# Optimization experiments

Hardware: AMD Instinct MI355X
Metric: run time of the kernel (lower is better)

## Reference

```python
import jax, jax.numpy as jnp
import numpy as np

B, T, D = 4, 2048, 768
H = 12
DH = D // H
DFF = 3072
EPS = 1e-5


def _layernorm(x, g, b):
    mu = jnp.mean(x, axis=-1, keepdims=True)
    var = jnp.var(x, axis=-1, keepdims=True)
    return (x - mu) * jax.lax.rsqrt(var + EPS) * g + b


def setup_inputs() -> dict:
    key = jax.random.key(0)
    ks = jax.random.split(key, 12)
    s = lambda fan_in: 1.0 / np.sqrt(fan_in)
    return {
        "x": jax.random.normal(ks[0], (B, T, D), dtype=jnp.float32),
        "ln1_g": jnp.ones((D,), jnp.float32),
        "ln1_b": jnp.zeros((D,), jnp.float32),
        "w_qkv": jax.random.uniform(ks[1], (D, 3 * D), jnp.float32, -s(D), s(D)),
        "b_qkv": jax.random.uniform(ks[2], (3 * D,), jnp.float32, -s(D), s(D)),
        "w_proj": jax.random.uniform(ks[3], (D, D), jnp.float32, -s(D), s(D)),
        "b_proj": jax.random.uniform(ks[4], (D,), jnp.float32, -s(D), s(D)),
        "ln2_g": jnp.ones((D,), jnp.float32),
        "ln2_b": jnp.zeros((D,), jnp.float32),
        "w_ff1": jax.random.uniform(ks[5], (D, DFF), jnp.float32, -s(D), s(D)),
        "b_ff1": jax.random.uniform(ks[6], (DFF,), jnp.float32, -s(D), s(D)),
        "w_ff2": jax.random.uniform(ks[7], (DFF, D), jnp.float32, -s(DFF), s(DFF)),
        "b_ff2": jax.random.uniform(ks[8], (D,), jnp.float32, -s(DFF), s(DFF)),
    }


def reference(x, ln1_g, ln1_b, w_qkv, b_qkv, w_proj, b_proj,
              ln2_g, ln2_b, w_ff1, b_ff1, w_ff2, b_ff2):
    # --- attention sublayer ---
    h = _layernorm(x, ln1_g, ln1_b)
    qkv = h @ w_qkv + b_qkv                       # [B,T,3D]
    q, k, v = jnp.split(qkv, 3, axis=-1)
    q = q.reshape(B, T, H, DH).transpose(0, 2, 1, 3)  # [B,H,T,DH]
    k = k.reshape(B, T, H, DH).transpose(0, 2, 1, 3)
    v = v.reshape(B, T, H, DH).transpose(0, 2, 1, 3)
    att = jnp.einsum('bhqd,bhkd->bhqk', q, k) / jnp.sqrt(jnp.float32(DH))
    causal = jnp.tril(jnp.ones((T, T), dtype=bool))
    att = jnp.where(causal, att, -jnp.inf)
    att = jax.nn.softmax(att, axis=-1)
    out = jnp.einsum('bhqk,bhkd->bhqd', att, v)    # [B,H,T,DH]
    out = out.transpose(0, 2, 1, 3).reshape(B, T, D)
    x = x + out @ w_proj + b_proj
    # --- MLP sublayer ---
    h2 = _layernorm(x, ln2_g, ln2_b)
    h2 = jax.nn.gelu(h2 @ w_ff1 + b_ff1, approximate=False)
    x = x + h2 @ w_ff2 + b_ff2
    return x
```

## Files before the change

### kernel.cpp

```cpp
#include <hip/hip_runtime.h>
#include <cstdint>
#include <cstddef>

typedef unsigned short u16;
typedef unsigned int u32;
typedef __attribute__((ext_vector_type(8))) short s16x8;
typedef __attribute__((ext_vector_type(4))) float f32x4;

#define NB 4
#define NT 2048
#define ND 768
#define NH 12
#define NDH 64
#define NFF 3072
#define NM (NB*NT)

__device__ __forceinline__ u16 f2b(float f){
  union { float f; unsigned u; } c; c.f = f;
  unsigned r = c.u + 0x7fffu + ((c.u >> 16) & 1u);
  return (u16)(r >> 16);
}

__device__ __forceinline__ f32x4 mfma16(s16x8 a, s16x8 b, f32x4 c){
  return __builtin_amdgcn_mfma_f32_16x16x32_bf16(a, b, c, 0, 0, 0);
}

__device__ __forceinline__ void stage16(u16* lds, const u16* g){
  __builtin_amdgcn_global_load_lds(
      (const __attribute__((address_space(1))) unsigned int*)g,
      (__attribute__((address_space(3))) unsigned int*)lds,
      16, 0, 0);
}

__device__ __forceinline__ float gelu_f(float v){
  const float x = v * 0.70710678118654752f;
  const float ax = fabsf(x);
  const float t = 1.f / (1.f + 0.3275911f * ax);
  const float y = t * (0.254829592f + t * (-0.284496736f + t * (1.421413741f
                + t * (-1.453152027f + t * 1.061405429f))));
  float er = 1.f - y * __expf(-ax * ax);
  er = copysignf(er, x);
  return 0.5f * v * (1.f + er);
}

__global__ __launch_bounds__(256) void transpose_bf16(
    const float* __restrict__ in, u16* __restrict__ out, int K, int N)
{
  __shared__ float tile[32][33];
  const int n0 = blockIdx.x * 32, k0 = blockIdx.y * 32;
  const int tx = threadIdx.x, ty = threadIdx.y;
  #pragma unroll
  for (int i = 0; i < 32; i += 8)
    tile[ty + i][tx] = in[(size_t)(k0 + ty + i) * N + n0 + tx];
  __syncthreads();
  #pragma unroll
  for (int i = 0; i < 32; i += 8)
    out[(size_t)(n0 + ty + i) * K + k0 + tx] = f2b(tile[tx][ty + i]);
}

__global__ __launch_bounds__(256) void ln_kernel(
    const float* __restrict__ x, const float* __restrict__ g,
    const float* __restrict__ b, u16* __restrict__ out)
{
  const int row = blockIdx.x;
  const int t = threadIdx.x;
  const float* xr = x + (size_t)row * ND;
  float v0 = xr[t], v1 = xr[t + 256], v2 = xr[t + 512];
  float s = v0 + v1 + v2;
  float ss = v0*v0 + v1*v1 + v2*v2;
  #pragma unroll
  for (int o = 32; o; o >>= 1) { s += __shfl_xor(s, o, 64); ss += __shfl_xor(ss, o, 64); }
  __shared__ float red[8];
  const int w = t >> 6;
  if ((t & 63) == 0) { red[w] = s; red[4 + w] = ss; }
  __syncthreads();
  s  = red[0] + red[1] + red[2] + red[3];
  ss = red[4] + red[5] + red[6] + red[7];
  const float mu = s * (1.f / ND);
  const float var = ss * (1.f / ND) - mu * mu;
  const float rinv = rsqrtf(var + 1e-5f);
  u16* orow = out + (size_t)row * ND;
  orow[t]       = f2b((v0 - mu) * rinv * g[t]       + b[t]);
  orow[t + 256] = f2b((v1 - mu) * rinv * g[t + 256] + b[t + 256]);
  orow[t + 512] = f2b((v2 - mu) * rinv * g[t + 512] + b[t + 512]);
}

template<int EPI>
__global__ __launch_bounds__(512, 2) void gemm256(
    const u16* __restrict__ A, const u16* __restrict__ Bt,
    const float* __restrict__ bias,
    void* __restrict__ o0, void* __restrict__ o1, void* __restrict__ o2,
    const int N, const int K)
{
  __shared__ u16 Al[2][16384];
  __shared__ u16 Bl[2][16384];
  const int tid = threadIdx.x;
  const int lane = tid & 63, wid = tid >> 6;
  const int wm = wid >> 2, wn = wid & 3;
  const int lg = lane >> 4, lm = lane & 15;

  const int nwg = gridDim.x * gridDim.y;
  int bid = blockIdx.y * gridDim.x + blockIdx.x;
  bid = (bid & 7) * (nwg >> 3) + (bid >> 3);
  const int bm = (bid % gridDim.x) * 256;
  const int bn = (bid / gridDim.x) * 256;

  f32x4 acc[8][4] = {};

  const int srow = (wid << 4) + (lane >> 2);
  const int schunk = (lane & 3) ^ ((lane >> 3) & 3);
  const u16* Ap = A  + (size_t)(bm + srow) * K + schunk * 8;
  const u16* Bp = Bt + (size_t)(bn + srow) * K + schunk * 8;
  const int wlds = wid << 9;

  const int nkt = K >> 6;

  auto STAGE = [&](int kt2) {
    const int buf = kt2 & 1;
    const size_t kof = (size_t)(kt2 << 6);
    #pragma unroll
    for (int h = 0; h < 2; ++h)
      #pragma unroll
      for (int L2 = 0; L2 < 2; ++L2) {
        const size_t gofs = (size_t)(L2 << 7) * K + kof + (h << 5);
        const int lofs = h * 8192 + L2 * 4096 + wlds;
        stage16(&Al[buf][lofs], Ap + gofs);
        stage16(&Bl[buf][lofs], Bp + gofs);
      }
  };

  auto LDA = [&](int buf, int rf, int ks) -> s16x8 {
    const int r = (wm << 7) + (rf << 4) + lm;
    const int s = lg ^ ((lm >> 1) & 3);
    return *(const s16x8*)&Al[buf][(ks << 13) + (r << 5) + (s << 3)];
  };
  auto LDB = [&](int buf, int cf, int ks) -> s16x8 {
    const int r = (wn << 6) + (cf << 4) + lm;
    const int s = lg ^ ((lm >> 1) & 3);
    return *(const s16x8*)&Bl[buf][(ks << 13) + (r << 5) + (s << 3)];
  };

  STAGE(0);

  for (int kt = 0; kt < nkt; ++kt) {
    const int buf = kt & 1;
    asm volatile("s_waitcnt vmcnt(0)" ::: "memory");
    __builtin_amdgcn_s_barrier();

    s16x8 a0[4][2], b0[2][2];
    #pragma unroll
    for (int i = 0; i < 4; ++i) { a0[i][0] = LDA(buf, i, 0); a0[i][1] = LDA(buf, i, 1); }
    #pragma unroll
    for (int j = 0; j < 2; ++j) { b0[j][0] = LDB(buf, j, 0); b0[j][1] = LDB(buf, j, 1); }
    if (kt + 1 < nkt) STAGE(kt + 1);
    __builtin_amdgcn_s_barrier();
    __builtin_amdgcn_s_setprio(1);
    #pragma unroll
    for (int i = 0; i < 4; ++i)
      #pragma unroll
      for (int j = 0; j < 2; ++j) {
        acc[i][j] = mfma16(a0[i][0], b0[j][0], acc[i][j]);
        acc[i][j] = mfma16(a0[i][1], b0[j][1], acc[i][j]);
      }
    __builtin_amdgcn_s_setprio(0);
    __builtin_amdgcn_s_barrier();

    s16x8 b1[2][2];
    #pragma unroll
    for (int j = 0; j < 2; ++j) { b1[j][0] = LDB(buf, 2 + j, 0); b1[j][1] = LDB(buf, 2 + j, 1); }
    __builtin_amdgcn_s_barrier();
    __builtin_amdgcn_s_setprio(1);
    #pragma unroll
    for (int i = 0; i < 4; ++i)
      #pragma unroll
      for (int j = 0; j < 2; ++j) {
        acc[i][2 + j] = mfma16(a0[i][0], b1[j][0], acc[i][2 + j]);
        acc[i][2 + j] = mfma16(a0[i][1], b1[j][1], acc[i][2 + j]);
      }
    __builtin_amdgcn_s_setprio(0);
    __builtin_amdgcn_s_barrier();

    s16x8 a1[4][2];
    #pragma unroll
    for (int i = 0; i < 4; ++i) { a1[i][0] = LDA(buf, 4 + i, 0); a1[i][1] = LDA(buf, 4 + i, 1); }
    __builtin_amdgcn_s_barrier();
    __builtin_amdgcn_s_setprio(1);
    #pragma unroll
    for (int i = 0; i < 4; ++i)
      #pragma unroll
      for (int j = 0; j < 2; ++j) {
        acc[4 + i][2 + j] = mfma16(a1[i][0], b1[j][0], acc[4 + i][2 + j]);
        acc[4 + i][2 + j] = mfma16(a1[i][1], b1[j][1], acc[4 + i][2 + j]);
      }
    __builtin_amdgcn_s_setprio(0);
    __builtin_amdgcn_s_barrier();

    __builtin_amdgcn_s_setprio(1);
    #pragma unroll
    for (int i = 0; i < 4; ++i)
      #pragma unroll
      for (int j = 0; j < 2; ++j) {
        acc[4 + i][j] = mfma16(a1[i][0], b0[j][0], acc[4 + i][j]);
        acc[4 + i][j] = mfma16(a1[i][1], b0[j][1], acc[4 + i][j]);
      }
    __builtin_amdgcn_s_setprio(0);
  }

  #pragma unroll
  for (int i = 0; i < 8; ++i)
    #pragma unroll
    for (int j = 0; j < 4; ++j) {
      const int col = bn + (wn << 6) + (j << 4) + lm;
      const float bb = bias[col];
      #pragma unroll
      for (int r = 0; r < 4; ++r) {
        const int row = bm + (wm << 7) + (i << 4) + (lg << 2) + r;
        float v = acc[i][j][r] + bb;
        if (EPI == 0) {
          u16* dst; int rem;
          if (col < ND)            { dst = (u16*)o0; rem = col; v *= 0.125f; }
          else if (col < 2 * ND)   { dst = (u16*)o1; rem = col - ND; }
          else                     { dst = (u16*)o2; rem = col - 2 * ND; }
          const int hh = rem >> 6, dh = rem & 63;
          const int bb2 = row >> 11, tt = row & 2047;
          dst[(((size_t)bb2 * NH + hh) * NT + tt) * NDH + dh] = f2b(v);
        } else {
          ((u16*)o0)[(size_t)row * NFF + col] = f2b(gelu_f(v));
        }
      }
    }
}

template<int EPI>
__global__ __launch_bounds__(256, 4) void gemm_bt(
    const u16* __restrict__ A, const u16* __restrict__ Bt,
    const float* __restrict__ bias, const float* __restrict__ res,
    void* __restrict__ o0, const int M, const int N, const int K)
{
  __shared__ u16 As[3][64 * 32];
  __shared__ u16 Bs[3][128 * 32];
  const int tid = threadIdx.x;
  const int lane = tid & 63, wid = tid >> 6;
  const int wr = wid >> 1, wc = wid & 1;
  const int lg = lane >> 4, lm = lane & 15;
  const int bm = blockIdx.x * 64, bn = blockIdx.y * 128;

  f32x4 acc[2][4] = {};

  const int srow = tid >> 2;
  const int schunk = (tid & 3) ^ ((tid >> 3) & 3);
  const u16* ApT = A  + (size_t)(bm + srow) * K + schunk * 8;
  const u16* BpT = Bt + (size_t)(bn + srow) * K + schunk * 8;
  const size_t rs64 = (size_t)64 * K;
  const int woff = wid * 512;
  const int fswz = (lm >> 1) & 3;

  const int nt = K >> 5;

  #pragma unroll
  for (int p = 0; p < 2; ++p) {
    const int k0 = p << 5;
    stage16(&As[p][woff], ApT + k0);
    stage16(&Bs[p][woff],        BpT + k0);
    stage16(&Bs[p][woff + 2048], BpT + rs64 + k0);
  }

  for (int t = 0; t < nt; ++t) {
    if (t < nt - 1) asm volatile("s_waitcnt vmcnt(3)" ::: "memory");
    else            asm volatile("s_waitcnt vmcnt(0)" ::: "memory");
    __builtin_amdgcn_s_barrier();
    __builtin_amdgcn_sched_barrier(0);
    if (t + 2 < nt) {
      const int k0 = (t + 2) << 5;
      const int wb = (t + 2) % 3;
      stage16(&As[wb][woff], ApT + k0);
      stage16(&Bs[wb][woff],        BpT + k0);
      stage16(&Bs[wb][woff + 2048], BpT + rs64 + k0);
    }
    __builtin_amdgcn_sched_barrier(0);
    const int rb = t % 3;
    s16x8 af[2], bf[4];
    #pragma unroll
    for (int i = 0; i < 2; i++)
      af[i] = *(const s16x8*)&As[rb][(wr * 32 + i * 16 + lm) * 32 + ((lg ^ fswz) * 8)];
    #pragma unroll
    for (int j = 0; j < 4; j++)
      bf[j] = *(const s16x8*)&Bs[rb][(wc * 64 + j * 16 + lm) * 32 + ((lg ^ fswz) * 8)];
    #pragma unroll
    for (int i = 0; i < 2; i++)
      #pragma unroll
      for (int j = 0; j < 4; j++)
        acc[i][j] = mfma16(af[i], bf[j], acc[i][j]);
  }

  #pragma unroll
  for (int i = 0; i < 2; i++)
    #pragma unroll
    for (int j = 0; j < 4; j++) {
      const int col = bn + wc * 64 + j * 16 + lm;
      const float bb = bias[col];
      #pragma unroll
      for (int r = 0; r < 4; r++) {
        const int row = bm + wr * 32 + i * 16 + lg * 4 + r;
        const float v = acc[i][j][r] + bb;
        ((float*)o0)[(size_t)row * ND + col] = v + res[(size_t)row * ND + col];
      }
    }
}

__global__ __launch_bounds__(256,2) void attn_kernel(
    const u16* __restrict__ Q, const u16* __restrict__ Kg,
    const u16* __restrict__ V, u16* __restrict__ O)
{
  const int pairIdx = blockIdx.y;
  const int bh = blockIdx.x;
  const int b = bh / NH, h = bh % NH;
  const int tid = threadIdx.x;
  const int lane = tid & 63, w = tid >> 6;
  const int lg = lane >> 4, lm = lane & 15;
  const int sr = tid >> 3;
  const int sc = (tid & 7) * 8;

  __shared__ u16 Ks[64 * 64];
  __shared__ u16 Vt[64 * 64];
  __shared__ u16 Ps[4][16 * 64];

  const u16* Qb = Q  + (size_t)bh * NT * NDH;
  const u16* Kb = Kg + (size_t)bh * NT * NDH;
  const u16* Vb = V  + (size_t)bh * NT * NDH;

  for (int half = 0; half < 2; ++half) {
    const int si = half ? (31 - pairIdx) : pairIdx;
    const int q0 = si * 64;
    const int ktmax = si;

    const s16x8 qf0 = *(const s16x8*)&Qb[(size_t)(q0 + w * 16 + lm) * NDH + lg * 8];
    const s16x8 qf1 = *(const s16x8*)&Qb[(size_t)(q0 + w * 16 + lm) * NDH + 32 + lg * 8];

    f32x4 oacc[4] = {};
    float m = -INFINITY, l = 0.f;

    s16x8 kva = *(const s16x8*)&Kb[(size_t)sr * NDH + sc];
    s16x8 kvb = *(const s16x8*)&Kb[(size_t)(sr + 32) * NDH + sc];
    s16x8 vva = *(const s16x8*)&Vb[(size_t)sr * NDH + sc];
    s16x8 vvb = *(const s16x8*)&Vb[(size_t)(sr + 32) * NDH + sc];

    for (int kt = 0; kt <= ktmax; ++kt) {
      __syncthreads();
      *(s16x8*)&Ks[sr * 64 + (sc ^ ((sr & 7) << 3))] = kva;
      *(s16x8*)&Ks[(sr + 32) * 64 + (sc ^ ((sr & 7) << 3))] = kvb;
      #pragma unroll
      for (int e = 0; e < 8; ++e)
        Vt[(sc + e) * 64 + (sr ^ ((tid & 7) << 3))] = (u16)vva[e];
      #pragma unroll
      for (int e = 0; e < 8; ++e)
        Vt[(sc + e) * 64 + ((sr + 32) ^ ((tid & 7) << 3))] = (u16)vvb[e];
      __syncthreads();

      if (kt < ktmax) {
        const u16* Kn = Kb + (size_t)(kt + 1) * 64 * NDH;
        const u16* Vn = Vb + (size_t)(kt + 1) * 64 * NDH;
        kva = *(const s16x8*)&Kn[(size_t)sr * NDH + sc];
        kvb = *(const s16x8*)&Kn[(size_t)(sr + 32) * NDH + sc];
        vva = *(const s16x8*)&Vn[(size_t)sr * NDH + sc];
        vvb = *(const s16x8*)&Vn[(size_t)(sr + 32) * NDH + sc];
      }

      f32x4 sv[4];
      #pragma unroll
      for (int n = 0; n < 4; ++n) {
        const int krow = (n * 16 + lm) * 64;
        const int swz = (lm & 7) << 3;
        s16x8 kf0 = *(const s16x8*)&Ks[krow + ((lg * 8) ^ swz)];
        s16x8 kf1 = *(const s16x8*)&Ks[krow + ((32 + lg * 8) ^ swz)];
        f32x4 s4 = {};
        s4 = mfma16(kf0, qf0, s4);
        s4 = mfma16(kf1, qf1, s4);
        sv[n] = s4;
      }

      if (kt == ktmax) {
        #pragma unroll
        for (int n = 0; n < 4; ++n)
          #pragma unroll
          for (int r = 0; r < 4; ++r)
            if (n * 16 + lg * 4 + r > w * 16 + lm) sv[n][r] = -INFINITY;
      }

      float mx = -INFINITY;
      #pragma unroll
      for (int n = 0; n < 4; ++n)
        #pragma unroll
        for (int r = 0; r < 4; ++r) mx = fmaxf(mx, sv[n][r]);
      mx = fmaxf(mx, __shfl_xor(mx, 16));
      mx = fmaxf(mx, __shfl_xor(mx, 32));
      const float mnew = fmaxf(m, mx);
      const float alpha = __expf(m - mnew);
      m = mnew;

      float rs = 0.f;
      u32 pk[4][2];
      #pragma unroll
      for (int n = 0; n < 4; ++n) {
        const float p0 = __expf(sv[n][0] - mnew);
        const float p1 = __expf(sv[n][1] - mnew);
        const float p2 = __expf(sv[n][2] - mnew);
        const float p3 = __expf(sv[n][3] - mnew);
        rs += (p0 + p1) + (p2 + p3);
        pk[n][0] = (u32)f2b(p0) | ((u32)f2b(p1) << 16);
        pk[n][1] = (u32)f2b(p2) | ((u32)f2b(p3) << 16);
      }
      rs += __shfl_xor(rs, 16);
      rs += __shfl_xor(rs, 32);
      l = l * alpha + rs;

      #pragma unroll
      for (int n = 0; n < 4; ++n) {
        const int idx0 = lm * 64 + ((n * 16 + lg * 4) ^ ((lm & 7) << 3));
        *(u32*)&Ps[w][idx0] = pk[n][0];
        *(u32*)&Ps[w][idx0 + 2] = pk[n][1];
      }

      float av[4];
      #pragma unroll
      for (int r = 0; r < 4; ++r) av[r] = __shfl(alpha, lg * 4 + r);
      #pragma unroll
      for (int d = 0; d < 4; ++d)
        #pragma unroll
        for (int r = 0; r < 4; ++r) oacc[d][r] *= av[r];

      #pragma unroll
      for (int kh = 0; kh < 2; ++kh) {
        const s16x8 pf = *(const s16x8*)&Ps[w][lm * 64 + ((kh * 32 + lg * 8) ^ ((lm & 7) << 3))];
        #pragma unroll
        for (int dt = 0; dt < 4; ++dt) {
          const int g = (2 * dt + (lm >> 3)) & 7;
          const s16x8 vf = *(const s16x8*)&Vt[(dt * 16 + lm) * 64 + (((kh * 4 + lg) ^ g) << 3)];
          oacc[dt] = mfma16(pf, vf, oacc[dt]);
        }
      }
    }

    float lv[4];
    #pragma unroll
    for (int r = 0; r < 4; ++r) lv[r] = 1.f / __shfl(l, lg * 4 + r);
    #pragma unroll
    for (int dt = 0; dt < 4; ++dt)
      #pragma unroll
      for (int r = 0; r < 4; ++r) {
        const int qg = q0 + w * 16 + lg * 4 + r;
        O[((size_t)b * NT + qg) * ND + h * NDH + dt * 16 + lm] = f2b(oacc[dt][r] * lv[r]);
      }
  }
}

extern "C" void kernel_launch(void* const* d_in, const int* in_sizes, int n_in,
                              void* d_out, int out_size, void* d_ws, size_t ws_size,
                              hipStream_t stream)
{
  const float* x      = (const float*)d_in[0];
  const float* ln1_g  = (const float*)d_in[1];
  const float* ln1_b  = (const float*)d_in[2];
  const float* w_qkv  = (const float*)d_in[3];
  const float* b_qkv  = (const float*)d_in[4];
  const float* w_proj = (const float*)d_in[5];
  const float* b_proj = (const float*)d_in[6];
  const float* ln2_g  = (const float*)d_in[7];
  const float* ln2_b  = (const float*)d_in[8];
  const float* w_ff1  = (const float*)d_in[9];
  const float* b_ff1  = (const float*)d_in[10];
  const float* w_ff2  = (const float*)d_in[11];
  const float* b_ff2  = (const float*)d_in[12];

  char* ws = (char*)d_ws;
  u16*   wt_qkv = (u16*)(ws + 0);
  u16*   wt_proj= (u16*)(ws + 3538944);
  u16*   wt_ff1 = (u16*)(ws + 4718592);
  u16*   wt_ff2 = (u16*)(ws + 9437184);
  u16*   hbuf   = (u16*)(ws + 14155776);
  u16*   qbuf   = (u16*)(ws + 26738688);
  u16*   kbuf   = (u16*)(ws + 39321600);
  u16*   vbuf   = (u16*)(ws + 51904512);
  u16*   aobuf  = (u16*)(ws + 64487424);
  float* x1     = (float*)(ws + 77070336);
  u16*   h2buf  = (u16*)(ws + 102236160);
  u16*   ff1buf = hbuf;

  transpose_bf16<<<dim3(2304/32,  768/32), dim3(32,8), 0, stream>>>(w_qkv,  wt_qkv,  768, 2304);
  transpose_bf16<<<dim3( 768/32,  768/32), dim3(32,8), 0, stream>>>(w_proj, wt_proj, 768,  768);
  transpose_bf16<<<dim3(3072/32,  768/32), dim3(32,8), 0, stream>>>(w_ff1,  wt_ff1,  768, 3072);
  transpose_bf16<<<dim3( 768/32, 3072/32), dim3(32,8), 0, stream>>>(w_ff2,  wt_ff2, 3072,  768);

  ln_kernel<<<NM, 256, 0, stream>>>(x, ln1_g, ln1_b, hbuf);
  gemm256<0><<<dim3(NM/256, 2304/256), 512, 0, stream>>>(hbuf, wt_qkv, b_qkv,
                                                         qbuf, kbuf, vbuf, 2304, ND);
  attn_kernel<<<dim3(NB*NH, 16), 256, 0, stream>>>(qbuf, kbuf, vbuf, aobuf);
  gemm_bt<1><<<dim3(NM/64, ND/128), 256, 0, stream>>>(aobuf, wt_proj, b_proj, x,
                                                      x1, NM, ND, ND);
  ln_kernel<<<NM, 256, 0, stream>>>(x1, ln2_g, ln2_b, h2buf);
  gemm256<2><<<dim3(NM/256, NFF/256), 512, 0, stream>>>(h2buf, wt_ff1, b_ff1,
                                                        ff1buf, nullptr, nullptr, NFF, ND);
  gemm_bt<3><<<dim3(NM/64, ND/128), 256, 0, stream>>>(ff1buf, wt_ff2, b_ff2, x1,
                                                      d_out, NM, ND, NFF);
}
```

Measured before the change: 339.8 us.

## Pipeline gemm256 staging per k-half, fuse weight transposes, fix Vt bank conflicts

The 256x256 GEMM main loop now splits each k-tile into two 32-wide halves. Global-to-LDS stages for A and B of the next tile are interleaved between MFMA phases, with partial vmcnt waits in place of a full drain each iteration. Bias values are preloaded before the loop. The four weight-transpose launches are merged into one kernel, and the attention V-transpose swizzle now folds in the element index to reduce LDS bank conflicts on stores and reads. Together these aim to cut load stalls, launch overhead and LDS conflicts, at the cost of more complex wait-count bookkeeping that must stay correct.

Result: faster. 326.5 us (-3.9%).

```diff
diff --git a/kernel.cpp b/kernel.cpp
--- a/kernel.cpp
+++ b/kernel.cpp
@@ -43,11 +43,21 @@
   return 0.5f * v * (1.f + er);
 }
 
-__global__ __launch_bounds__(256) void transpose_bf16(
-    const float* __restrict__ in, u16* __restrict__ out, int K, int N)
+__global__ __launch_bounds__(256) void transpose_all(
+    const float* __restrict__ w_qkv, const float* __restrict__ w_proj,
+    const float* __restrict__ w_ff1, const float* __restrict__ w_ff2,
+    u16* __restrict__ o_qkv, u16* __restrict__ o_proj,
+    u16* __restrict__ o_ff1, u16* __restrict__ o_ff2)
 {
+  int bid = blockIdx.x;
+  const float* in; u16* out; int K, N, nx;
+  if (bid < 1728)      { in = w_qkv;  out = o_qkv;  K = 768;  N = 2304; nx = 72; }
+  else if ((bid -= 1728) < 576)  { in = w_proj; out = o_proj; K = 768;  N = 768;  nx = 24; }
+  else if ((bid -= 576) < 2304)  { in = w_ff1;  out = o_ff1;  K = 768;  N = 3072; nx = 96; }
+  else { bid -= 2304;              in = w_ff2;  out = o_ff2;  K = 3072; N = 768;  nx = 24; }
+  const int n0 = (bid % nx) * 32, k0 = (bid / nx) * 32;
+
   __shared__ float tile[32][33];
-  const int n0 = blockIdx.x * 32, k0 = blockIdx.y * 32;
   const int tx = threadIdx.x, ty = threadIdx.y;
   #pragma unroll
   for (int i = 0; i < 32; i += 8)
@@ -115,20 +125,18 @@
 
   const int nkt = K >> 6;
 
-  auto STAGE = [&](int kt2) {
+  auto STAGE_A = [&](int kt2, int h) {
     const int buf = kt2 & 1;
-    const size_t kof = (size_t)(kt2 << 6);
-    #pragma unroll
-    for (int h = 0; h < 2; ++h)
-      #pragma unroll
-      for (int L2 = 0; L2 < 2; ++L2) {
-        const size_t gofs = (size_t)(L2 << 7) * K + kof + (h << 5);
-        const int lofs = h * 8192 + L2 * 4096 + wlds;
-        stage16(&Al[buf][lofs], Ap + gofs);
-        stage16(&Bl[buf][lofs], Bp + gofs);
-      }
+    const size_t kof = (size_t)(kt2 << 6) + (h << 5);
+    stage16(&Al[buf][h * 8192 + wlds],        Ap + kof);
+    stage16(&Al[buf][h * 8192 + 4096 + wlds], Ap + (size_t)128 * K + kof);
   };
-
+  auto STAGE_B = [&](int kt2, int h) {
+    const int buf = kt2 & 1;
+    const size_t kof = (size_t)(kt2 << 6) + (h << 5);
+    stage16(&Bl[buf][h * 8192 + wlds],        Bp + kof);
+    stage16(&Bl[buf][h * 8192 + 4096 + wlds], Bp + (size_t)128 * K + kof);
+  };
   auto LDA = [&](int buf, int rf, int ks) -> s16x8 {
     const int r = (wm << 7) + (rf << 4) + lm;
     const int s = lg ^ ((lm >> 1) & 3);
@@ -140,70 +148,79 @@
     return *(const s16x8*)&Bl[buf][(ks << 13) + (r << 5) + (s << 3)];
   };
 
-  STAGE(0);
+  float bb[4];
+  #pragma unroll
+  for (int j = 0; j < 4; ++j) bb[j] = bias[bn + (wn << 6) + (j << 4) + lm];
+  asm volatile("s_waitcnt vmcnt(0)" ::: "memory");
+
+  STAGE_A(0, 0); STAGE_B(0, 0); STAGE_A(0, 1); STAGE_B(0, 1);
+  asm volatile("s_waitcnt vmcnt(4)" ::: "memory");
+  __builtin_amdgcn_s_barrier();
+  __builtin_amdgcn_sched_barrier(0);
 
   for (int kt = 0; kt < nkt; ++kt) {
     const int buf = kt & 1;
-    asm volatile("s_waitcnt vmcnt(0)" ::: "memory");
-    __builtin_amdgcn_s_barrier();
-
-    s16x8 a0[4][2], b0[2][2];
-    #pragma unroll
-    for (int i = 0; i < 4; ++i) { a0[i][0] = LDA(buf, i, 0); a0[i][1] = LDA(buf, i, 1); }
-    #pragma unroll
-    for (int j = 0; j < 2; ++j) { b0[j][0] = LDB(buf, j, 0); b0[j][1] = LDB(buf, j, 1); }
-    if (kt + 1 < nkt) STAGE(kt + 1);
+    const bool more = (kt + 1 < nkt);
+    s16x8 a[8], b0, b1;
+
+    #pragma unroll
+    for (int i = 0; i < 8; ++i) a[i] = LDA(buf, i, 0);
+    b0 = LDB(buf, 0, 0); b1 = LDB(buf, 1, 0);
+    if (more) STAGE_A(kt + 1, 0);
     __builtin_amdgcn_s_barrier();
     __builtin_amdgcn_s_setprio(1);
     #pragma unroll
-    for (int i = 0; i < 4; ++i)
-      #pragma unroll
-      for (int j = 0; j < 2; ++j) {
-        acc[i][j] = mfma16(a0[i][0], b0[j][0], acc[i][j]);
-        acc[i][j] = mfma16(a0[i][1], b0[j][1], acc[i][j]);
-      }
+    for (int i = 0; i < 8; ++i) {
+      acc[i][0] = mfma16(a[i], b0, acc[i][0]);
+      acc[i][1] = mfma16(a[i], b1, acc[i][1]);
+    }
     __builtin_amdgcn_s_setprio(0);
     __builtin_amdgcn_s_barrier();
 
-    s16x8 b1[2][2];
-    #pragma unroll
-    for (int j = 0; j < 2; ++j) { b1[j][0] = LDB(buf, 2 + j, 0); b1[j][1] = LDB(buf, 2 + j, 1); }
+    b0 = LDB(buf, 2, 0); b1 = LDB(buf, 3, 0);
+    if (more) STAGE_B(kt + 1, 0);
     __builtin_amdgcn_s_barrier();
     __builtin_amdgcn_s_setprio(1);
     #pragma unroll
-    for (int i = 0; i < 4; ++i)
-      #pragma unroll
-      for (int j = 0; j < 2; ++j) {
-        acc[i][2 + j] = mfma16(a0[i][0], b1[j][0], acc[i][2 + j]);
-        acc[i][2 + j] = mfma16(a0[i][1], b1[j][1], acc[i][2 + j]);
-      }
+    for (int i = 0; i < 8; ++i) {
+      acc[i][2] = mfma16(a[i], b0, acc[i][2]);
+      acc[i][3] = mfma16(a[i], b1, acc[i][3]);
+    }
     __builtin_amdgcn_s_setprio(0);
-    __builtin_amdgcn_s_barrier();
-
-    s16x8 a1[4][2];
-    #pragma unroll
-    for (int i = 0; i < 4; ++i) { a1[i][0] = LDA(buf, 4 + i, 0); a1[i][1] = LDA(buf, 4 + i, 1); }
+    if (more) asm volatile("s_waitcnt vmcnt(4)" ::: "memory");
+    else      asm volatile("s_waitcnt vmcnt(0)" ::: "memory");
+    __builtin_amdgcn_s_barrier();
+    __builtin_amdgcn_sched_barrier(0);
+
+    #pragma unroll
+    for (int i = 0; i < 8; ++i) a[i] = LDA(buf, i, 1);
+    b0 = LDB(buf, 0, 1); b1 = LDB(buf, 1, 1);
+    if (more) STAGE_A(kt + 1, 1);
     __builtin_amdgcn_s_barrier();
     __builtin_amdgcn_s_setprio(1);
     #pragma unroll
-    for (int i = 0; i < 4; ++i)
-      #pragma unroll
-      for (int j = 0; j < 2; ++j) {
-        acc[4 + i][2 + j] = mfma16(a1[i][0], b1[j][0], acc[4 + i][2 + j]);
-        acc[4 + i][2 + j] = mfma16(a1[i][1], b1[j][1], acc[4 + i][2 + j]);
-      }
+    for (int i = 0; i < 8; ++i) {
+      acc[i][0] = mfma16(a[i], b0, acc[i][0]);
+      acc[i][1] = mfma16(a[i], b1, acc[i][1]);
+    }
     __builtin_amdgcn_s_setprio(0);
     __builtin_amdgcn_s_barrier();
 
+    b0 = LDB(buf, 2, 1); b1 = LDB(buf, 3, 1);
+    if (more) STAGE_B(kt + 1, 1);
+    __builtin_amdgcn_s_barrier();
     __builtin_amdgcn_s_setprio(1);
     #pragma unroll
-    for (int i = 0; i < 4; ++i)
-      #pragma unroll
-      for (int j = 0; j < 2; ++j) {
-        acc[4 + i][j] = mfma16(a1[i][0], b0[j][0], acc[4 + i][j]);
-        acc[4 + i][j] = mfma16(a1[i][1], b0[j][1], acc[4 + i][j]);
-      }
+    for (int i = 0; i < 8; ++i) {
+      acc[i][2] = mfma16(a[i], b0, acc[i][2]);
+      acc[i][3] = mfma16(a[i], b1, acc[i][3]);
+    }
     __builtin_amdgcn_s_setprio(0);
+    if (more) {
+      asm volatile("s_waitcnt vmcnt(4)" ::: "memory");
+      __builtin_amdgcn_s_barrier();
+      __builtin_amdgcn_sched_barrier(0);
+    }
   }
 
   #pragma unroll
@@ -211,11 +228,10 @@
     #pragma unroll
     for (int j = 0; j < 4; ++j) {
       const int col = bn + (wn << 6) + (j << 4) + lm;
-      const float bb = bias[col];
       #pragma unroll
       for (int r = 0; r < 4; ++r) {
         const int row = bm + (wm << 7) + (i << 4) + (lg << 2) + r;
-        float v = acc[i][j][r] + bb;
+        float v = acc[i][j][r] + bb[j];
         if (EPI == 0) {
           u16* dst; int rem;
           if (col < ND)            { dst = (u16*)o0; rem = col; v *= 0.125f; }
@@ -298,11 +314,11 @@
     #pragma unroll
     for (int j = 0; j < 4; j++) {
       const int col = bn + wc * 64 + j * 16 + lm;
-      const float bb = bias[col];
+      const float bbv = bias[col];
       #pragma unroll
       for (int r = 0; r < 4; r++) {
         const int row = bm + wr * 32 + i * 16 + lg * 4 + r;
-        const float v = acc[i][j][r] + bb;
+        const float v = acc[i][j][r] + bbv;
         ((float*)o0)[(size_t)row * ND + col] = v + res[(size_t)row * ND + col];
       }
     }
@@ -351,10 +367,10 @@
       *(s16x8*)&Ks[(sr + 32) * 64 + (sc ^ ((sr & 7) << 3))] = kvb;
       #pragma unroll
       for (int e = 0; e < 8; ++e)
-        Vt[(sc + e) * 64 + (sr ^ ((tid & 7) << 3))] = (u16)vva[e];
+        Vt[(sc + e) * 64 + (sr ^ ((((tid & 7) ^ e)) << 3))] = (u16)vva[e];
       #pragma unroll
       for (int e = 0; e < 8; ++e)
-        Vt[(sc + e) * 64 + ((sr + 32) ^ ((tid & 7) << 3))] = (u16)vvb[e];
+        Vt[(sc + e) * 64 + ((sr + 32) ^ ((((tid & 7) ^ e)) << 3))] = (u16)vvb[e];
       __syncthreads();
 
       if (kt < ktmax) {
@@ -434,7 +450,7 @@
         const s16x8 pf = *(const s16x8*)&Ps[w][lm * 64 + ((kh * 32 + lg * 8) ^ ((lm & 7) << 3))];
         #pragma unroll
         for (int dt = 0; dt < 4; ++dt) {
-          const int g = (2 * dt + (lm >> 3)) & 7;
+          const int g = ((2 * dt + (lm >> 3)) ^ (lm & 7)) & 7;
           const s16x8 vf = *(const s16x8*)&Vt[(dt * 16 + lm) * 64 + (((kh * 4 + lg) ^ g) << 3)];
           oacc[dt] = mfma16(pf, vf, oacc[dt]);
         }
@@ -486,10 +502,8 @@
   u16*   h2buf  = (u16*)(ws + 102236160);
   u16*   ff1buf = hbuf;
 
-  transpose_bf16<<<dim3(2304/32,  768/32), dim3(32,8), 0, stream>>>(w_qkv,  wt_qkv,  768, 2304);
-  transpose_bf16<<<dim3( 768/32,  768/32), dim3(32,8), 0, stream>>>(w_proj, wt_proj, 768,  768);
-  transpose_bf16<<<dim3(3072/32,  768/32), dim3(32,8), 0, stream>>>(w_ff1,  wt_ff1,  768, 3072);
-  transpose_bf16<<<dim3( 768/32, 3072/32), dim3(32,8), 0, stream>>>(w_ff2,  wt_ff2, 3072,  768);
+  transpose_all<<<6912, dim3(32,8), 0, stream>>>(w_qkv, w_proj, w_ff1, w_ff2,
+                                                 wt_qkv, wt_proj, wt_ff1, wt_ff2);
 
   ln_kernel<<<NM, 256, 0, stream>>>(x, ln1_g, ln1_b, hbuf);
   gemm256<0><<<dim3(NM/256, 2304/256), 512, 0, stream>>>(hbuf, wt_qkv, b_qkv,
```
